# Optimization experiments

Hardware: AMD Instinct MI355X
Metric: run time of the kernel (lower is better)

Reference implementation:

```python
import jax, jax.numpy as jnp
import numpy as np
from jax import lax

N = 256        # graph nodes (== conv5 channels)
C = 128        # diff-pool clusters
E = 4096       # number of edges
EPS = 1e-15    # PyG dense_diff_pool entropy eps


def setup_inputs():
    key = jax.random.key(0)
    ks = jax.random.split(key, 24)
    def rn(k, shape, scale):
        return jax.random.normal(k, shape, dtype=jnp.float32) * scale
    inp = {
        "inputs": jax.random.normal(ks[0], (1, 3, 512, 512), dtype=jnp.float32),
        "edge_index": jax.random.randint(ks[1], (2, E), 0, N, dtype=jnp.int32),
    }
    convs = [(3, 32), (32, 64), (64, 128), (128, 256), (256, 256)]
    for i, (ci, co) in enumerate(convs):
        inp[f"w{i+1}"] = rn(ks[2 + i], (co, ci, 3, 3), 0.05)
        inp[f"b{i+1}"] = jnp.zeros((co,), jnp.float32)
    sages = [(256, 2), (256, 128), (2, 2)]
    for i, (ci, co) in enumerate(sages):
        inp[f"s{i+1}_wl"] = rn(ks[10 + 3 * i], (ci, co), 0.1)
        inp[f"s{i+1}_wr"] = rn(ks[11 + 3 * i], (ci, co), 0.1)
        inp[f"s{i+1}_b"] = jnp.zeros((co,), jnp.float32)
    return inp


def _conv_block(x, w, b):
    # 3x3 SAME conv -> relu -> 2x2 max pool (stride 2), NCHW layout
    x = lax.conv_general_dilated(x, w, (1, 1), 'SAME',
                                 dimension_numbers=('NCHW', 'OIHW', 'NCHW'))
    x = jax.nn.relu(x + b[None, :, None, None])
    return lax.reduce_window(x, -jnp.inf, lax.max,
                             (1, 1, 2, 2), (1, 1, 2, 2), 'VALID')


def _sage(x, src, dst, wl, wr, b, n):
    # PyG SAGEConv(normalize=False): lin_l(mean_{src->dst} x_src) + lin_r(x)
    tot = jax.ops.segment_sum(x[src], dst, num_segments=n)
    cnt = jax.ops.segment_sum(jnp.ones((dst.shape[0],), x.dtype), dst, num_segments=n)
    agg = jnp.where(cnt[:, None] > 0, tot / jnp.maximum(cnt, 1.0)[:, None], 0.0)
    return agg @ wl + b + x @ wr


def reference(inputs, edge_index, w1, b1, w2, b2, w3, b3, w4, b4, w5, b5,
              s1_wl, s1_wr, s1_b, s2_wl, s2_wr, s2_b, s3_wl, s3_wr, s3_b):
    x = inputs
    for w, b in ((w1, b1), (w2, b2), (w3, b3), (w4, b4), (w5, b5)):
        x = _conv_block(x, w, b)
    org = x.reshape(N, N)  # (256 channels, 16*16 spatial) -> node features
    src, dst = edge_index[0], edge_index[1]
    x1 = _sage(org, src, dst, s1_wl, s1_wr, s1_b, N)  # (256, 2)
    s = _sage(org, src, dst, s2_wl, s2_wr, s2_b, N)   # (256, 128)
    # dense adjacency (duplicate edges accumulate, matching scipy coo.todense())
    adj = jnp.zeros((N, N), org.dtype).at[src, dst].add(1.0)
    # dense_diff_pool
    s_soft = jax.nn.softmax(s, axis=-1)
    x_pool = s_soft.T @ x1               # (128, 2)
    adj_pool = s_soft.T @ adj @ s_soft   # (128, 128)
    link_loss = jnp.linalg.norm(adj - s_soft @ s_soft.T) / (N * N)
    ent_loss = (-s_soft * jnp.log(s_soft + EPS)).sum(-1).mean()
    nodes = jnp.tanh(x_pool)             # (128, 2)
    # per-row argmax-equality thresholding (vectorized: rows are independent)
    row_max = adj_pool.max(axis=1, keepdims=True)
    edge_bin = (adj_pool == row_max).astype(org.dtype)  # (128, 128)
    # sage3 over the binarized dense adjacency (equivalent to dense_to_sparse + SAGEConv)
    indeg = edge_bin.sum(axis=0)
    agg = jnp.where(indeg[:, None] > 0,
                    (edge_bin.T @ nodes) / jnp.maximum(indeg, 1.0)[:, None], 0.0)
    out = agg @ s3_wl + s3_b + nodes @ s3_wr  # (128, 2)
    return out.reshape(-1), link_loss, ent_loss, nodes, edge_bin
```

## Files before the change

kernel.cpp:

```cpp
#include <hip/hip_runtime.h>
#include <math.h>

#define NN 256
#define NE 4096
#define NC 128

using short8  = __attribute__((ext_vector_type(8))) short;
using short4v = __attribute__((ext_vector_type(4))) short;
using f32x4   = __attribute__((ext_vector_type(4))) float;

static __device__ __forceinline__ unsigned short f2bf(float x) {
    unsigned u = __float_as_uint(x);
    unsigned r = (u + 0x7FFF + ((u >> 16) & 1)) >> 16;
    return (unsigned short)r;
}

static __device__ __forceinline__ float block_sum_256(float v, float* red4) {
    #pragma unroll
    for (int o = 32; o > 0; o >>= 1) v += __shfl_xor(v, o);
    __syncthreads();
    if ((threadIdx.x & 63) == 0) red4[threadIdx.x >> 6] = v;
    __syncthreads();
    return (red4[0] + red4[1]) + (red4[2] + red4[3]);
}

__global__ void prep_kernel(const float* __restrict__ w1, const float* __restrict__ w2,
                            const float* __restrict__ w3, const float* __restrict__ w4,
                            const float* __restrict__ w5,
                            unsigned short* __restrict__ f1, unsigned short* __restrict__ f2,
                            unsigned short* __restrict__ f3, unsigned short* __restrict__ f4,
                            unsigned short* __restrict__ f5,
                            const int* __restrict__ src, const int* __restrict__ dst,
                            float* __restrict__ adj, float* __restrict__ adjT)
{
    int b = blockIdx.x;
    int tid = threadIdx.x;
    if (b >= 478) {
        __shared__ int cntA[256], cntT[256];
        const int n = b - 478;
        cntA[tid] = 0; cntT[tid] = 0;
        __syncthreads();
        #pragma unroll
        for (int i = 0; i < 16; ++i) {
            int e = tid + i * 256;
            int s = src[e], d = dst[e];
            if (s == n) atomicAdd(&cntA[d], 1);
            if (d == n) atomicAdd(&cntT[s], 1);
        }
        __syncthreads();
        adj[n * NN + tid]  = (float)cntA[tid];
        adjT[n * NN + tid] = (float)cntT[tid];
        return;
    }
    if (b == 477) {
        int lane = tid & 63, rest = tid >> 6;
        int g = rest & 1, slot = rest >> 1;
        int oc = g * 16 + (lane & 15);
        short8 v;
        #pragma unroll
        for (int j = 0; j < 8; ++j) {
            int k = (lane >> 4) * 8 + j;
            float wv = 0.f;
            if (slot == 0) {
                int tap = k >> 2, ch = k & 3;
                if (ch < 3) wv = w1[oc * 27 + ch * 9 + tap];
            } else {
                if (k < 3) wv = w1[oc * 27 + k * 9 + 8];
            }
            v[j] = (short)f2bf(wv);
        }
        *(short8*)&f1[(size_t)tid * 8] = v;
        return;
    }
    const float* w; unsigned short* f; int CIN, NG, NCH, base;
    if (b < 9)        { w = w2; f = f2; CIN = 32;  NG = 4;  NCH = 1; base = 0;   }
    else if (b < 45)  { w = w3; f = f3; CIN = 64;  NG = 8;  NCH = 2; base = 9;   }
    else if (b < 189) { w = w4; f = f4; CIN = 128; NG = 16; NCH = 4; base = 45;  }
    else              { w = w5; f = f5; CIN = 256; NG = 16; NCH = 8; base = 189; }
    int idx = (b - base) * 256 + tid;
    int lane = idx & 63, rest = idx >> 6;
    int c = rest % NCH; rest /= NCH;
    int g = rest % NG;  int t = rest / NG;
    if (t >= 9) return;
    int oc = g * 16 + (lane & 15);
    int cin0 = c * 32 + (lane >> 4) * 8;
    short8 v;
    #pragma unroll
    for (int j = 0; j < 8; ++j) {
        v[j] = (short)f2bf(w[((size_t)oc * CIN + cin0 + j) * 9 + t]);
    }
    *(short8*)&f[(size_t)idx * 8] = v;
}

__global__ __launch_bounds__(256) void conv1_kernel(
    const float* __restrict__ in, const unsigned short* __restrict__ wf1,
    const float* __restrict__ bias, unsigned short* __restrict__ out)
{
    constexpr int Hc = 512;
    const int tid = threadIdx.x;
    const int lane = tid & 63, wid = tid >> 6;
    const int col = lane & 15, kgl = lane >> 4;
    const int X0 = blockIdx.x * 16, Y0 = blockIdx.y * 16;
    __shared__ __align__(16) unsigned short lds[18][18][4];
    for (int i = tid; i < 324; i += 256) {
        int hy = i / 18, hx = i - hy * 18;
        int gy = Y0 + hy - 1, gx = X0 + hx - 1;
        float v0 = 0.f, v1 = 0.f, v2 = 0.f;
        if (gy >= 0 && gy < Hc && gx >= 0 && gx < Hc) {
            v0 = in[0 * 262144 + gy * 512 + gx];
            v1 = in[1 * 262144 + gy * 512 + gx];
            v2 = in[2 * 262144 + gy * 512 + gx];
        }
        uint2 uu;
        uu.x = f2bf(v0) | ((unsigned)f2bf(v1) << 16);
        uu.y = f2bf(v2);
        *(uint2*)&lds[hy][hx][0] = uu;
    }
    short8 af[2][2];
    #pragma unroll
    for (int slot = 0; slot < 2; ++slot) {
        #pragma unroll
        for (int g = 0; g < 2; ++g) {
            af[slot][g] = *(const short8*)&wf1[((size_t)((slot * 2 + g) * 64 + lane)) * 8];
        }
    }
    __syncthreads();
    f32x4 acc[2][4];
    #pragma unroll
    for (int g = 0; g < 2; ++g) {
        #pragma unroll
        for (int r = 0; r < 4; ++r) acc[g][r] = {0.f, 0.f, 0.f, 0.f};
    }
    const int t0 = 2 * kgl, t1 = 2 * kgl + 1;
    const int dy0 = t0 / 3, dx0 = t0 % 3, dy1 = t1 / 3, dx1 = t1 % 3;
    #pragma unroll
    for (int r = 0; r < 4; ++r) {
        const int py = wid * 4 + r;
        short4v lo = *(const short4v*)&lds[py + dy0][col + dx0][0];
        short4v hi = *(const short4v*)&lds[py + dy1][col + dx1][0];
        short8 bf0 = __builtin_shufflevector(lo, hi, 0, 1, 2, 3, 4, 5, 6, 7);
        short4v z4 = {0, 0, 0, 0};
        short4v t8 = z4;
        if (kgl == 0) t8 = *(const short4v*)&lds[py + 2][col + 2][0];
        short8 bf1 = __builtin_shufflevector(t8, z4, 0, 1, 2, 3, 4, 5, 6, 7);
        #pragma unroll
        for (int g = 0; g < 2; ++g) {
            acc[g][r] = __builtin_amdgcn_mfma_f32_16x16x32_bf16(af[0][g], bf0, acc[g][r], 0, 0, 0);
            acc[g][r] = __builtin_amdgcn_mfma_f32_16x16x32_bf16(af[1][g], bf1, acc[g][r], 0, 0, 0);
        }
    }
    #pragma unroll
    for (int g = 0; g < 2; ++g) {
        const int oc = g * 16 + kgl * 4;
        const float4 bb = *(const float4*)&bias[oc];
        const float bbv[4] = {bb.x, bb.y, bb.z, bb.w};
        #pragma unroll
        for (int pr = 0; pr < 2; ++pr) {
            float vv[4];
            #pragma unroll
            for (int q = 0; q < 4; ++q) {
                float v = fmaxf(acc[g][2 * pr][q], acc[g][2 * pr + 1][q]);
                v = fmaxf(v, __shfl_xor(v, 1));
                vv[q] = fmaxf(v + bbv[q], 0.f);
            }
            if (!(col & 1)) {
                unsigned u0 = f2bf(vv[0]) | ((unsigned)f2bf(vv[1]) << 16);
                unsigned u1 = f2bf(vv[2]) | ((unsigned)f2bf(vv[3]) << 16);
                const int pry = Y0 / 2 + wid * 2 + pr;
                const int prx = X0 / 2 + (col >> 1);
                uint2 uu; uu.x = u0; uu.y = u1;
                *(uint2*)&out[((size_t)(pry * 256 + prx)) * 32 + oc] = uu;
            }
        }
    }
}

template<int CIN, int COUT, int Hc, int OCB, int CSPLIT>
__global__ __launch_bounds__(256) void conv_mfma(
    const unsigned short* __restrict__ in, const unsigned short* __restrict__ wfrag,
    const float* __restrict__ bias, void* __restrict__ outv)
{
    constexpr int TR = 8;
    constexpr int NOG = OCB / 16;
    constexpr int NG  = COUT / 16;
    constexpr int NCHT = CIN / 32;
    constexpr int NCH = NCHT / CSPLIT;
    constexpr int RPW = 2;
    constexpr int ITEMS = (TR + 2) * 18 * 4;
    constexpr int NIT = 3;
    const int tid = threadIdx.x;
    const int lane = tid & 63, wid = tid >> 6;
    const int col = lane & 15, kgl = lane >> 4;
    const int X0 = blockIdx.x * 16, Y0 = blockIdx.y * TR;
    const int ob = blockIdx.z / CSPLIT, cs = blockIdx.z % CSPLIT;

    __shared__ __align__(16) unsigned short lds[2][ITEMS * 8];

    int ioff[NIT]; bool ival[NIT]; int loff[NIT];
    #pragma unroll
    for (int it = 0; it < NIT; ++it) {
        int i = tid + it * 256;
        int kg = i & 3, rem = i >> 2;
        int hx = rem % 18, hy = rem / 18;
        int gy = Y0 + hy - 1, gx = X0 + hx - 1;
        ival[it] = (i < ITEMS) && gy >= 0 && gy < Hc && gx >= 0 && gx < Hc;
        ioff[it] = (gy * Hc + gx) * CIN + kg * 8;
        loff[it] = ((hy * 4 + kg) * 18 + hx) * 8;
    }
    short8 sreg[NIT];
    auto sload = [&](int ca) {
        #pragma unroll
        for (int it = 0; it < NIT; ++it) {
            short8 v = {0, 0, 0, 0, 0, 0, 0, 0};
            if (ival[it]) v = *(const short8*)&in[ioff[it] + ca * 32];
            sreg[it] = v;
        }
    };
    auto swrite = [&](int buf) {
        #pragma unroll
        for (int it = 0; it < NIT; ++it) {
            if (tid + it * 256 < ITEMS) *(short8*)&lds[buf][loff[it]] = sreg[it];
        }
    };

    f32x4 acc[NOG][RPW];
    #pragma unroll
    for (int g = 0; g < NOG; ++g) {
        #pragma unroll
        for (int r = 0; r < RPW; ++r) acc[g][r] = {0.f, 0.f, 0.f, 0.f};
    }

    sload(cs * NCH);
    swrite(0);
    __syncthreads();
    for (int cc = 0; cc < NCH; ++cc) {
        const int ca = cs * NCH + cc;
        if (cc + 1 < NCH) sload(ca + 1);
        const unsigned short* L = &lds[cc & 1][0];
        #pragma unroll
        for (int t = 0; t < 9; ++t) {
            const int ky = t / 3, kx = t % 3;
            short8 af[NOG];
            #pragma unroll
            for (int g = 0; g < NOG; ++g) {
                af[g] = *(const short8*)&wfrag[((((size_t)t * NG + ob * NOG + g) * NCHT + ca) * 64 + lane) * 8];
            }
            #pragma unroll
            for (int r = 0; r < RPW; ++r) {
                const int py = wid * RPW + r;
                short8 bf = *(const short8*)&L[(((py + ky) * 4 + kgl) * 18 + col + kx) * 8];
                #pragma unroll
                for (int g = 0; g < NOG; ++g) {
                    acc[g][r] = __builtin_amdgcn_mfma_f32_16x16x32_bf16(af[g], bf, acc[g][r], 0, 0, 0);
                }
            }
        }
        if (cc + 1 < NCH) { swrite((cc + 1) & 1); __syncthreads(); }
    }

    if constexpr (CSPLIT == 1) {
        constexpr int Wp = Hc / 2;
        unsigned short* outp = (unsigned short*)outv;
        #pragma unroll
        for (int g = 0; g < NOG; ++g) {
            const int oc = (ob * NOG + g) * 16 + kgl * 4;
            const float4 bb = *(const float4*)&bias[oc];
            const float bbv[4] = {bb.x, bb.y, bb.z, bb.w};
            float vv[4];
            #pragma unroll
            for (int q = 0; q < 4; ++q) {
                float v = fmaxf(acc[g][0][q], acc[g][1][q]);
                v = fmaxf(v, __shfl_xor(v, 1));
                vv[q] = fmaxf(v + bbv[q], 0.f);
            }
            if (!(col & 1)) {
                unsigned u0 = f2bf(vv[0]) | ((unsigned)f2bf(vv[1]) << 16);
                unsigned u1 = f2bf(vv[2]) | ((unsigned)f2bf(vv[3]) << 16);
                const int pry = Y0 / 2 + wid;
                const int prx = X0 / 2 + (col >> 1);
                uint2 uu; uu.x = u0; uu.y = u1;
                *(uint2*)&outp[((size_t)(pry * Wp + prx)) * COUT + oc] = uu;
            }
        }
    } else {
        float* po = (float*)outv;
        #pragma unroll
        for (int g = 0; g < NOG; ++g) {
            #pragma unroll
            for (int r = 0; r < RPW; ++r) {
                const int gy = Y0 + wid * RPW + r;
                #pragma unroll
                for (int q = 0; q < 4; ++q) {
                    const int oc = (ob * NOG + g) * 16 + kgl * 4 + q;
                    po[((size_t)(cs * COUT + oc) * Hc + gy) * Hc + X0 + col] = acc[g][r][q];
                }
            }
        }
    }
}

template<int COUT, int HP, int CS>
__global__ void finalize_pool(const float* __restrict__ partial, const float* __restrict__ bias,
                              float* __restrict__ out)
{
    int idx = blockIdx.x * 256 + threadIdx.x;
    if (idx >= COUT * HP * HP) return;
    constexpr int H = HP * 2;
    int x = idx & (HP - 1); int rest = idx / HP;
    int y = rest & (HP - 1); int oc = rest / HP;
    float v00 = 0.f, v01 = 0.f, v10 = 0.f, v11 = 0.f;
    #pragma unroll
    for (int cs = 0; cs < CS; ++cs) {
        const float* p = partial + ((size_t)(cs * COUT + oc) * H + 2 * y) * H + 2 * x;
        v00 += p[0]; v01 += p[1]; v10 += p[H]; v11 += p[H + 1];
    }
    float m = fmaxf(fmaxf(v00, v01), fmaxf(v10, v11)) + bias[oc];
    out[idx] = fmaxf(m, 0.f);
}


__global__ __launch_bounds__(256) void node_fused_kernel(
    const float* __restrict__ adjT, const float* __restrict__ org,
    const float* __restrict__ s1wl, const float* __restrict__ s1wr, const float* __restrict__ s1b,
    const float* __restrict__ s2wl, const float* __restrict__ s2wr, const float* __restrict__ s2b,
    float* __restrict__ s_soft, float* __restrict__ s_softT,
    float* __restrict__ x1g, float* __restrict__ entp)
{
    int n = blockIdx.x, t = threadIdx.x;
    __shared__ float rowT[256], orgn[256], aggn[256], red[256], sm[128], red4[4];
    float rT = adjT[n * 256 + t];
    rowT[t] = rT; orgn[t] = org[n * 256 + t];
    __syncthreads();
    float cnt = block_sum_256(rT, red4);
    float a0 = 0.f, a1 = 0.f, a2 = 0.f, a3 = 0.f;
    #pragma unroll 8
    for (int s = 0; s < 256; s += 4) {
        a0 = fmaf(rowT[s + 0], org[(s + 0) * 256 + t], a0);
        a1 = fmaf(rowT[s + 1], org[(s + 1) * 256 + t], a1);
        a2 = fmaf(rowT[s + 2], org[(s + 2) * 256 + t], a2);
        a3 = fmaf(rowT[s + 3], org[(s + 3) * 256 + t], a3);
    }
    float acc = (a0 + a1) + (a2 + a3);
    float aggv = (cnt > 0.f) ? acc / cnt : 0.f;
    aggn[t] = aggv;
    float orgv = orgn[t];
    float x10 = block_sum_256(aggv * s1wl[2 * t] + orgv * s1wr[2 * t], red4) + s1b[0];
    float x11 = block_sum_256(aggv * s1wl[2 * t + 1] + orgv * s1wr[2 * t + 1], red4) + s1b[1];
    if (t == 0) { x1g[n * 2 + 0] = x10; x1g[n * 2 + 1] = x11; }
    int p = t & 127, h = t >> 7;
    float b0 = 0.f, b1 = 0.f, b2 = 0.f, b3 = 0.f;
    #pragma unroll 8
    for (int k = h * 128; k < h * 128 + 128; k += 2) {
        b0 = fmaf(aggn[k],     s2wl[k * NC + p],       b0);
        b1 = fmaf(orgn[k],     s2wr[k * NC + p],       b1);
        b2 = fmaf(aggn[k + 1], s2wl[(k + 1) * NC + p], b2);
        b3 = fmaf(orgn[k + 1], s2wr[(k + 1) * NC + p], b3);
    }
    red[t] = (b0 + b1) + (b2 + b3);
    __syncthreads();
    if (t < 128) sm[p] = red[t] + red[t + 128] + s2b[p];
    __syncthreads();
    if (t < 128) red[t] = sm[t];
    __syncthreads();
    for (int s = 64; s > 0; s >>= 1) { if (t < s) red[t] = fmaxf(red[t], red[t + s]); __syncthreads(); }
    float mx = red[0];
    __syncthreads();
    float e = 0.f;
    if (t < 128) { e = expf(sm[t] - mx); red[t] = e; } else { red[t] = 0.f; }
    __syncthreads();
    for (int s = 64; s > 0; s >>= 1) { if (t < s) red[t] += red[t + s]; __syncthreads(); }
    float denom = red[0];
    float q = e / denom;
    if (t < 128) {
        s_soft[n * NC + t] = q;
        s_softT[t * 256 + n] = q;
    }
    float ev = (t < 128) ? -q * logf(q + 1e-15f) : 0.f;
    float esum = block_sum_256(ev, red4);
    if (t == 0) entp[n] = esum;
}

__global__ __launch_bounds__(256) void row_fused_kernel(
    const float* __restrict__ adj, const float* __restrict__ s_soft,
    const float* __restrict__ s_softT, float* __restrict__ T, float* __restrict__ lpart)
{
    int i = blockIdx.x, j = threadIdx.x;
    __shared__ float si[NC], adjrow[256], tbuf[256], red4[4];
    adjrow[j] = adj[i * 256 + j];
    if (j < NC) si[j] = s_soft[i * NC + j];
    __syncthreads();
    float d0 = 0.f, d1 = 0.f, d2 = 0.f, d3 = 0.f;
    #pragma unroll 8
    for (int k = 0; k < NC; k += 4) {
        d0 = fmaf(si[k + 0], s_softT[(k + 0) * 256 + j], d0);
        d1 = fmaf(si[k + 1], s_softT[(k + 1) * 256 + j], d1);
        d2 = fmaf(si[k + 2], s_softT[(k + 2) * 256 + j], d2);
        d3 = fmaf(si[k + 3], s_softT[(k + 3) * 256 + j], d3);
    }
    float dot = (d0 + d1) + (d2 + d3);
    float dd = adjrow[j] - dot;
    float lsum = block_sum_256(dd * dd, red4);
    if (j == 0) lpart[i] = lsum;
    int p = j & 127, h = j >> 7;
    float a0 = 0.f, a1 = 0.f;
    #pragma unroll 8
    for (int k = h * 128; k < h * 128 + 128; k += 2) {
        a0 = fmaf(adjrow[k],     s_soft[k * NC + p],       a0);
        a1 = fmaf(adjrow[k + 1], s_soft[(k + 1) * NC + p], a1);
    }
    tbuf[j] = a0 + a1;
    __syncthreads();
    if (j < 128) T[i * NC + j] = tbuf[j] + tbuf[j + 128];
}

__global__ __launch_bounds__(256) void cluster_fused_kernel(
    const float* __restrict__ s_softT, const float* __restrict__ T, const float* __restrict__ x1g,
    float* __restrict__ eb_out, float* __restrict__ nodes_out)
{
    int c = blockIdx.x, t = threadIdx.x;
    __shared__ float colc[256], red[256], ap[NC], red4[4];
    colc[t] = s_softT[c * 256 + t];
    __syncthreads();
    int p = t & 127, h = t >> 7;
    float a0 = 0.f, a1 = 0.f;
    #pragma unroll 8
    for (int n = h * 128; n < h * 128 + 128; n += 2) {
        a0 = fmaf(colc[n],     T[n * NC + p],       a0);
        a1 = fmaf(colc[n + 1], T[(n + 1) * NC + p], a1);
    }
    red[t] = a0 + a1;
    __syncthreads();
    if (t < 128) ap[t] = red[t] + red[t + 128];
    __syncthreads();
    if (t < 128) red[t] = ap[t];
    __syncthreads();
    for (int s = 64; s > 0; s >>= 1) { if (t < s) red[t] = fmaxf(red[t], red[t + s]); __syncthreads(); }
    float mx = red[0];
    if (t < 128) eb_out[c * NC + t] = (ap[t] == mx) ? 1.f : 0.f;
    float n0 = tanhf(block_sum_256(colc[t] * x1g[t * 2 + 0], red4));
    float n1 = tanhf(block_sum_256(colc[t] * x1g[t * 2 + 1], red4));
    if (t == 0) { nodes_out[c * 2 + 0] = n0; nodes_out[c * 2 + 1] = n1; }
}

__global__ __launch_bounds__(256) void final_kernel(
    const float* __restrict__ lpart, const float* __restrict__ entp,
    const float* __restrict__ eb, const float* __restrict__ nodes,
    const float* __restrict__ wl, const float* __restrict__ wr, const float* __restrict__ b,
    float* __restrict__ out_main, float* __restrict__ out_link, float* __restrict__ out_ent)
{
    int t = threadIdx.x;
    __shared__ float red4[4];
    float ls = block_sum_256(lpart[t], red4);
    if (t == 0) out_link[0] = sqrtf(ls) / (float)(NN * NN);
    float es = block_sum_256(entp[t], red4);
    if (t == 0) out_ent[0] = es / (float)NN;
    if (t < NC) {
        int j = t;
        float i0 = 0.f, i1 = 0.f, a00 = 0.f, a01 = 0.f, a10 = 0.f, a11 = 0.f;
        #pragma unroll 8
        for (int i2 = 0; i2 < NC; i2 += 2) {
            float e0 = eb[i2 * NC + j];
            float e1 = eb[(i2 + 1) * NC + j];
            i0 += e0; i1 += e1;
            a00 = fmaf(e0, nodes[i2 * 2 + 0], a00);
            a01 = fmaf(e0, nodes[i2 * 2 + 1], a01);
            a10 = fmaf(e1, nodes[(i2 + 1) * 2 + 0], a10);
            a11 = fmaf(e1, nodes[(i2 + 1) * 2 + 1], a11);
        }
        float indeg = i0 + i1;
        float a0 = a00 + a10, a1 = a01 + a11;
        float inv = (indeg > 0.f) ? 1.f / fmaxf(indeg, 1.f) : 0.f;
        float g0 = a0 * inv, g1 = a1 * inv;
        float n0 = nodes[j * 2 + 0], n1 = nodes[j * 2 + 1];
        out_main[j * 2 + 0] = g0 * wl[0] + g1 * wl[2] + b[0] + n0 * wr[0] + n1 * wr[2];
        out_main[j * 2 + 1] = g0 * wl[1] + g1 * wl[3] + b[1] + n0 * wr[1] + n1 * wr[3];
    }
}

extern "C" void kernel_launch(void* const* d_in, const int* in_sizes, int n_in,
                              void* d_out, int out_size, void* d_ws, size_t ws_size,
                              hipStream_t stream)
{
    const float* input = (const float*)d_in[0];
    const int* eidx = (const int*)d_in[1];
    const int* src = eidx;
    const int* dst = eidx + NE;
    const float* w1 = (const float*)d_in[2];  const float* b1 = (const float*)d_in[3];
    const float* w2 = (const float*)d_in[4];  const float* b2 = (const float*)d_in[5];
    const float* w3 = (const float*)d_in[6];  const float* b3 = (const float*)d_in[7];
    const float* w4 = (const float*)d_in[8];  const float* b4 = (const float*)d_in[9];
    const float* w5 = (const float*)d_in[10]; const float* b5 = (const float*)d_in[11];
    const float* s1_wl = (const float*)d_in[12]; const float* s1_wr = (const float*)d_in[13];
    const float* s1_b  = (const float*)d_in[14];
    const float* s2_wl = (const float*)d_in[15]; const float* s2_wr = (const float*)d_in[16];
    const float* s2_b  = (const float*)d_in[17];
    const float* s3_wl = (const float*)d_in[18]; const float* s3_wr = (const float*)d_in[19];
    const float* s3_b  = (const float*)d_in[20];

    float* ws = (float*)d_ws;
    unsigned short* c1 = (unsigned short*)(ws);
    unsigned short* c2 = (unsigned short*)(ws + 1048576);
    unsigned short* c3 = (unsigned short*)(ws);
    unsigned short* c4 = (unsigned short*)(ws + 1048576);
    float* P5  = ws;
    float* ORG = ws + 1179648;
    unsigned short* f1 = (unsigned short*)(ws + 1572864);
    unsigned short* f2 = (unsigned short*)(ws + 1573888);
    unsigned short* f3 = (unsigned short*)(ws + 1583104);
    unsigned short* f4 = (unsigned short*)(ws + 1619968);
    unsigned short* f5 = (unsigned short*)(ws + 1767424);
    float* adj     = ws + 2062336;
    float* adjT    = ws + 2127872;
    float* s_soft  = ws + 2193408;
    float* T       = ws + 2226176;
    float* x1g     = ws + 2258944;
    float* lpart   = ws + 2259456;
    float* entp    = ws + 2259712;
    float* s_softT = ws + 2259968;

    float* fout = (float*)d_out;
    float* out_main  = fout;
    float* out_link  = fout + 256;
    float* out_ent   = fout + 257;
    float* out_nodes = fout + 258;
    float* out_eb    = fout + 514;

    prep_kernel<<<734, 256, 0, stream>>>(w1, w2, w3, w4, w5, f1, f2, f3, f4, f5,
                                         src, dst, adj, adjT);
    conv1_kernel<<<dim3(32, 32), 256, 0, stream>>>(input, f1, b1, c1);
    conv_mfma<32,  64, 256, 64, 1><<<dim3(16, 32, 1), 256, 0, stream>>>(c1, f2, b2, c2);
    conv_mfma<64, 128, 128, 64, 1><<<dim3(8, 16, 2),  256, 0, stream>>>(c2, f3, b3, c3);
    conv_mfma<128, 256, 64, 32, 1><<<dim3(4, 8, 8),   256, 0, stream>>>(c3, f4, b4, c4);
    conv_mfma<256, 256, 32, 16, 2><<<dim3(2, 4, 32),  256, 0, stream>>>(c4, f5, b5, P5);
    finalize_pool<256, 16, 2><<<256, 256, 0, stream>>>(P5, b5, ORG);

    node_fused_kernel<<<256, 256, 0, stream>>>(adjT, ORG, s1_wl, s1_wr, s1_b,
                                               s2_wl, s2_wr, s2_b, s_soft, s_softT, x1g, entp);
    row_fused_kernel<<<256, 256, 0, stream>>>(adj, s_soft, s_softT, T, lpart);
    cluster_fused_kernel<<<128, 256, 0, stream>>>(s_softT, T, x1g, out_eb, out_nodes);
    final_kernel<<<1, 256, 0, stream>>>(lpart, entp, out_eb, out_nodes,
                                        s3_wl, s3_wr, s3_b, out_main, out_link, out_ent);
}
```

Before: 107.7 us.

## Merge all stages into one cooperative persistent kernel with grid syncs

Replaces the eleven separate kernel launches with a single cooperative kernel of 256 blocks. Each stage loops over its former block indices and the stages are separated by grid-wide syncs. Shared memory becomes one union buffer reused by every stage. The goal is to remove per-launch overhead and inter-kernel gaps, at the cost of fixed parallelism (256 blocks, so conv1's 1024 tiles are serialized four per block), grid.sync overhead, and lower occupancy per stage.

```diff
diff --git a/kernel.cpp b/kernel.cpp
--- a/kernel.cpp
+++ b/kernel.cpp
@@ -1,5 +1,8 @@
 #include <hip/hip_runtime.h>
+#include <hip/hip_cooperative_groups.h>
 #include <math.h>
+
+namespace cg = cooperative_groups;
 
 #define NN 256
 #define NE 4096
@@ -24,32 +27,35 @@
     return (red4[0] + red4[1]) + (red4[2] + red4[3]);
 }
 
-__global__ void prep_kernel(const float* __restrict__ w1, const float* __restrict__ w2,
-                            const float* __restrict__ w3, const float* __restrict__ w4,
-                            const float* __restrict__ w5,
-                            unsigned short* __restrict__ f1, unsigned short* __restrict__ f2,
-                            unsigned short* __restrict__ f3, unsigned short* __restrict__ f4,
-                            unsigned short* __restrict__ f5,
-                            const int* __restrict__ src, const int* __restrict__ dst,
-                            float* __restrict__ adj, float* __restrict__ adjT)
-{
-    int b = blockIdx.x;
+struct MegaArgs {
+    const float* input; const int* src; const int* dst;
+    const float *w1, *b1, *w2, *b2, *w3, *b3, *w4, *b4, *w5, *b5;
+    const float *s1wl, *s1wr, *s1b, *s2wl, *s2wr, *s2b, *s3wl, *s3wr, *s3b;
+    unsigned short *c1, *c2, *c3, *c4, *f1, *f2, *f3, *f4, *f5;
+    float *P5, *ORG, *adj, *adjT, *s_soft, *s_softT, *T, *x1g, *lpart, *entp;
+    float *out_main, *out_link, *out_ent, *out_nodes, *out_eb;
+};
+
+static __device__ void prep_item(int b, const MegaArgs& a, int* icnt)
+{
     int tid = threadIdx.x;
     if (b >= 478) {
-        __shared__ int cntA[256], cntT[256];
+        int* cntA = icnt; int* cntT = icnt + 256;
         const int n = b - 478;
+        __syncthreads();
         cntA[tid] = 0; cntT[tid] = 0;
         __syncthreads();
         #pragma unroll
         for (int i = 0; i < 16; ++i) {
             int e = tid + i * 256;
-            int s = src[e], d = dst[e];
+            int s = a.src[e], d = a.dst[e];
             if (s == n) atomicAdd(&cntA[d], 1);
             if (d == n) atomicAdd(&cntT[s], 1);
         }
         __syncthreads();
-        adj[n * NN + tid]  = (float)cntA[tid];
-        adjT[n * NN + tid] = (float)cntT[tid];
+        a.adj[n * NN + tid]  = (float)cntA[tid];
+        a.adjT[n * NN + tid] = (float)cntT[tid];
+        __syncthreads();
         return;
     }
     if (b == 477) {
@@ -63,20 +69,20 @@
             float wv = 0.f;
             if (slot == 0) {
                 int tap = k >> 2, ch = k & 3;
-                if (ch < 3) wv = w1[oc * 27 + ch * 9 + tap];
+                if (ch < 3) wv = a.w1[oc * 27 + ch * 9 + tap];
             } else {
-                if (k < 3) wv = w1[oc * 27 + k * 9 + 8];
+                if (k < 3) wv = a.w1[oc * 27 + k * 9 + 8];
             }
             v[j] = (short)f2bf(wv);
         }
-        *(short8*)&f1[(size_t)tid * 8] = v;
+        *(short8*)&a.f1[(size_t)tid * 8] = v;
         return;
     }
     const float* w; unsigned short* f; int CIN, NG, NCH, base;
-    if (b < 9)        { w = w2; f = f2; CIN = 32;  NG = 4;  NCH = 1; base = 0;   }
-    else if (b < 45)  { w = w3; f = f3; CIN = 64;  NG = 8;  NCH = 2; base = 9;   }
-    else if (b < 189) { w = w4; f = f4; CIN = 128; NG = 16; NCH = 4; base = 45;  }
-    else              { w = w5; f = f5; CIN = 256; NG = 16; NCH = 8; base = 189; }
+    if (b < 9)        { w = a.w2; f = a.f2; CIN = 32;  NG = 4;  NCH = 1; base = 0;   }
+    else if (b < 45)  { w = a.w3; f = a.f3; CIN = 64;  NG = 8;  NCH = 2; base = 9;   }
+    else if (b < 189) { w = a.w4; f = a.f4; CIN = 128; NG = 16; NCH = 4; base = 45;  }
+    else              { w = a.w5; f = a.f5; CIN = 256; NG = 16; NCH = 8; base = 189; }
     int idx = (b - base) * 256 + tid;
     int lane = idx & 63, rest = idx >> 6;
     int c = rest % NCH; rest /= NCH;
@@ -92,36 +98,34 @@
     *(short8*)&f[(size_t)idx * 8] = v;
 }
 
-__global__ __launch_bounds__(256) void conv1_kernel(
-    const float* __restrict__ in, const unsigned short* __restrict__ wf1,
-    const float* __restrict__ bias, unsigned short* __restrict__ out)
+static __device__ void conv1_tile(int bx, int by, const MegaArgs& a, unsigned short* ldsb)
 {
     constexpr int Hc = 512;
     const int tid = threadIdx.x;
     const int lane = tid & 63, wid = tid >> 6;
     const int col = lane & 15, kgl = lane >> 4;
-    const int X0 = blockIdx.x * 16, Y0 = blockIdx.y * 16;
-    __shared__ __align__(16) unsigned short lds[18][18][4];
+    const int X0 = bx * 16, Y0 = by * 16;
+    __syncthreads();
     for (int i = tid; i < 324; i += 256) {
         int hy = i / 18, hx = i - hy * 18;
         int gy = Y0 + hy - 1, gx = X0 + hx - 1;
         float v0 = 0.f, v1 = 0.f, v2 = 0.f;
         if (gy >= 0 && gy < Hc && gx >= 0 && gx < Hc) {
-            v0 = in[0 * 262144 + gy * 512 + gx];
-            v1 = in[1 * 262144 + gy * 512 + gx];
-            v2 = in[2 * 262144 + gy * 512 + gx];
+            v0 = a.input[0 * 262144 + gy * 512 + gx];
+            v1 = a.input[1 * 262144 + gy * 512 + gx];
+            v2 = a.input[2 * 262144 + gy * 512 + gx];
         }
         uint2 uu;
         uu.x = f2bf(v0) | ((unsigned)f2bf(v1) << 16);
         uu.y = f2bf(v2);
-        *(uint2*)&lds[hy][hx][0] = uu;
+        *(uint2*)&ldsb[(size_t)i * 4] = uu;
     }
     short8 af[2][2];
     #pragma unroll
     for (int slot = 0; slot < 2; ++slot) {
         #pragma unroll
         for (int g = 0; g < 2; ++g) {
-            af[slot][g] = *(const short8*)&wf1[((size_t)((slot * 2 + g) * 64 + lane)) * 8];
+            af[slot][g] = *(const short8*)&a.f1[((size_t)((slot * 2 + g) * 64 + lane)) * 8];
         }
     }
     __syncthreads();
@@ -136,12 +140,12 @@
     #pragma unroll
     for (int r = 0; r < 4; ++r) {
         const int py = wid * 4 + r;
-        short4v lo = *(const short4v*)&lds[py + dy0][col + dx0][0];
-        short4v hi = *(const short4v*)&lds[py + dy1][col + dx1][0];
+        short4v lo = *(const short4v*)&ldsb[((py + dy0) * 18 + col + dx0) * 4];
+        short4v hi = *(const short4v*)&ldsb[((py + dy1) * 18 + col + dx1) * 4];
         short8 bf0 = __builtin_shufflevector(lo, hi, 0, 1, 2, 3, 4, 5, 6, 7);
         short4v z4 = {0, 0, 0, 0};
         short4v t8 = z4;
-        if (kgl == 0) t8 = *(const short4v*)&lds[py + 2][col + 2][0];
+        if (kgl == 0) t8 = *(const short4v*)&ldsb[((py + 2) * 18 + col + 2) * 4];
         short8 bf1 = __builtin_shufflevector(t8, z4, 0, 1, 2, 3, 4, 5, 6, 7);
         #pragma unroll
         for (int g = 0; g < 2; ++g) {
@@ -152,7 +156,7 @@
     #pragma unroll
     for (int g = 0; g < 2; ++g) {
         const int oc = g * 16 + kgl * 4;
-        const float4 bb = *(const float4*)&bias[oc];
+        const float4 bb = *(const float4*)&a.b1[oc];
         const float bbv[4] = {bb.x, bb.y, bb.z, bb.w};
         #pragma unroll
         for (int pr = 0; pr < 2; ++pr) {
@@ -169,16 +173,16 @@
                 const int pry = Y0 / 2 + wid * 2 + pr;
                 const int prx = X0 / 2 + (col >> 1);
                 uint2 uu; uu.x = u0; uu.y = u1;
-                *(uint2*)&out[((size_t)(pry * 256 + prx)) * 32 + oc] = uu;
+                *(uint2*)&a.c1[((size_t)(pry * 256 + prx)) * 32 + oc] = uu;
             }
         }
     }
 }
 
 template<int CIN, int COUT, int Hc, int OCB, int CSPLIT>
-__global__ __launch_bounds__(256) void conv_mfma(
+static __device__ void conv_tile(int bx, int by, int bz,
     const unsigned short* __restrict__ in, const unsigned short* __restrict__ wfrag,
-    const float* __restrict__ bias, void* __restrict__ outv)
+    const float* __restrict__ bias, void* __restrict__ outv, unsigned short* ldsb)
 {
     constexpr int TR = 8;
     constexpr int NOG = OCB / 16;
@@ -191,10 +195,8 @@
     const int tid = threadIdx.x;
     const int lane = tid & 63, wid = tid >> 6;
     const int col = lane & 15, kgl = lane >> 4;
-    const int X0 = blockIdx.x * 16, Y0 = blockIdx.y * TR;
-    const int ob = blockIdx.z / CSPLIT, cs = blockIdx.z % CSPLIT;
-
-    __shared__ __align__(16) unsigned short lds[2][ITEMS * 8];
+    const int X0 = bx * 16, Y0 = by * TR;
+    const int ob = bz / CSPLIT, cs = bz % CSPLIT;
 
     int ioff[NIT]; bool ival[NIT]; int loff[NIT];
     #pragma unroll
@@ -219,7 +221,7 @@
     auto swrite = [&](int buf) {
         #pragma unroll
         for (int it = 0; it < NIT; ++it) {
-            if (tid + it * 256 < ITEMS) *(short8*)&lds[buf][loff[it]] = sreg[it];
+            if (tid + it * 256 < ITEMS) *(short8*)&ldsb[buf * (ITEMS * 8) + loff[it]] = sreg[it];
         }
     };
 
@@ -230,13 +232,14 @@
         for (int r = 0; r < RPW; ++r) acc[g][r] = {0.f, 0.f, 0.f, 0.f};
     }
 
+    __syncthreads();
     sload(cs * NCH);
     swrite(0);
     __syncthreads();
     for (int cc = 0; cc < NCH; ++cc) {
         const int ca = cs * NCH + cc;
         if (cc + 1 < NCH) sload(ca + 1);
-        const unsigned short* L = &lds[cc & 1][0];
+        const unsigned short* L = &ldsb[(cc & 1) * (ITEMS * 8)];
         #pragma unroll
         for (int t = 0; t < 9; ++t) {
             const int ky = t / 3, kx = t % 3;
@@ -299,66 +302,59 @@
     }
 }
 
-template<int COUT, int HP, int CS>
-__global__ void finalize_pool(const float* __restrict__ partial, const float* __restrict__ bias,
-                              float* __restrict__ out)
-{
-    int idx = blockIdx.x * 256 + threadIdx.x;
-    if (idx >= COUT * HP * HP) return;
-    constexpr int H = HP * 2;
+static __device__ void finalize_item(int b, const MegaArgs& a)
+{
+    constexpr int HP = 16, H = 32, CS = 2, COUT = 256;
+    int idx = b * 256 + threadIdx.x;
     int x = idx & (HP - 1); int rest = idx / HP;
     int y = rest & (HP - 1); int oc = rest / HP;
     float v00 = 0.f, v01 = 0.f, v10 = 0.f, v11 = 0.f;
     #pragma unroll
     for (int cs = 0; cs < CS; ++cs) {
-        const float* p = partial + ((size_t)(cs * COUT + oc) * H + 2 * y) * H + 2 * x;
+        const float* p = a.P5 + ((size_t)(cs * COUT + oc) * H + 2 * y) * H + 2 * x;
         v00 += p[0]; v01 += p[1]; v10 += p[H]; v11 += p[H + 1];
     }
-    float m = fmaxf(fmaxf(v00, v01), fmaxf(v10, v11)) + bias[oc];
-    out[idx] = fmaxf(m, 0.f);
-}
-
-
-__global__ __launch_bounds__(256) void node_fused_kernel(
-    const float* __restrict__ adjT, const float* __restrict__ org,
-    const float* __restrict__ s1wl, const float* __restrict__ s1wr, const float* __restrict__ s1b,
-    const float* __restrict__ s2wl, const float* __restrict__ s2wr, const float* __restrict__ s2b,
-    float* __restrict__ s_soft, float* __restrict__ s_softT,
-    float* __restrict__ x1g, float* __restrict__ entp)
-{
-    int n = blockIdx.x, t = threadIdx.x;
-    __shared__ float rowT[256], orgn[256], aggn[256], red[256], sm[128], red4[4];
-    float rT = adjT[n * 256 + t];
-    rowT[t] = rT; orgn[t] = org[n * 256 + t];
+    float m = fmaxf(fmaxf(v00, v01), fmaxf(v10, v11)) + a.b5[oc];
+    a.ORG[idx] = fmaxf(m, 0.f);
+}
+
+static __device__ void node_tile(int n, const MegaArgs& a, float* sf)
+{
+    int t = threadIdx.x;
+    float* rowT = sf; float* orgn = sf + 256; float* aggn = sf + 512;
+    float* red = sf + 768; float* sm = sf + 1024; float* red4 = sf + 1152;
+    __syncthreads();
+    float rT = a.adjT[n * 256 + t];
+    rowT[t] = rT; orgn[t] = a.ORG[n * 256 + t];
     __syncthreads();
     float cnt = block_sum_256(rT, red4);
     float a0 = 0.f, a1 = 0.f, a2 = 0.f, a3 = 0.f;
     #pragma unroll 8
     for (int s = 0; s < 256; s += 4) {
-        a0 = fmaf(rowT[s + 0], org[(s + 0) * 256 + t], a0);
-        a1 = fmaf(rowT[s + 1], org[(s + 1) * 256 + t], a1);
-        a2 = fmaf(rowT[s + 2], org[(s + 2) * 256 + t], a2);
-        a3 = fmaf(rowT[s + 3], org[(s + 3) * 256 + t], a3);
+        a0 = fmaf(rowT[s + 0], a.ORG[(s + 0) * 256 + t], a0);
+        a1 = fmaf(rowT[s + 1], a.ORG[(s + 1) * 256 + t], a1);
+        a2 = fmaf(rowT[s + 2], a.ORG[(s + 2) * 256 + t], a2);
+        a3 = fmaf(rowT[s + 3], a.ORG[(s + 3) * 256 + t], a3);
     }
     float acc = (a0 + a1) + (a2 + a3);
     float aggv = (cnt > 0.f) ? acc / cnt : 0.f;
     aggn[t] = aggv;
     float orgv = orgn[t];
-    float x10 = block_sum_256(aggv * s1wl[2 * t] + orgv * s1wr[2 * t], red4) + s1b[0];
-    float x11 = block_sum_256(aggv * s1wl[2 * t + 1] + orgv * s1wr[2 * t + 1], red4) + s1b[1];
-    if (t == 0) { x1g[n * 2 + 0] = x10; x1g[n * 2 + 1] = x11; }
+    float x10 = block_sum_256(aggv * a.s1wl[2 * t] + orgv * a.s1wr[2 * t], red4) + a.s1b[0];
+    float x11 = block_sum_256(aggv * a.s1wl[2 * t + 1] + orgv * a.s1wr[2 * t + 1], red4) + a.s1b[1];
+    if (t == 0) { a.x1g[n * 2 + 0] = x10; a.x1g[n * 2 + 1] = x11; }
     int p = t & 127, h = t >> 7;
     float b0 = 0.f, b1 = 0.f, b2 = 0.f, b3 = 0.f;
     #pragma unroll 8
     for (int k = h * 128; k < h * 128 + 128; k += 2) {
-        b0 = fmaf(aggn[k],     s2wl[k * NC + p],       b0);
-        b1 = fmaf(orgn[k],     s2wr[k * NC + p],       b1);
-        b2 = fmaf(aggn[k + 1], s2wl[(k + 1) * NC + p], b2);
-        b3 = fmaf(orgn[k + 1], s2wr[(k + 1) * NC + p], b3);
+        b0 = fmaf(aggn[k],     a.s2wl[k * NC + p],       b0);
+        b1 = fmaf(orgn[k],     a.s2wr[k * NC + p],       b1);
+        b2 = fmaf(aggn[k + 1], a.s2wl[(k + 1) * NC + p], b2);
+        b3 = fmaf(orgn[k + 1], a.s2wr[(k + 1) * NC + p], b3);
     }
     red[t] = (b0 + b1) + (b2 + b3);
     __syncthreads();
-    if (t < 128) sm[p] = red[t] + red[t + 128] + s2b[p];
+    if (t < 128) sm[p] = red[t] + red[t + 128] + a.s2b[p];
     __syncthreads();
     if (t < 128) red[t] = sm[t];
     __syncthreads();
@@ -372,61 +368,59 @@
     float denom = red[0];
     float q = e / denom;
     if (t < 128) {
-        s_soft[n * NC + t] = q;
-        s_softT[t * 256 + n] = q;
+        a.s_soft[n * NC + t] = q;
+        a.s_softT[t * 256 + n] = q;
     }
     float ev = (t < 128) ? -q * logf(q + 1e-15f) : 0.f;
     float esum = block_sum_256(ev, red4);
-    if (t == 0) entp[n] = esum;
-}
-
-__global__ __launch_bounds__(256) void row_fused_kernel(
-    const float* __restrict__ adj, const float* __restrict__ s_soft,
-    const float* __restrict__ s_softT, float* __restrict__ T, float* __restrict__ lpart)
-{
-    int i = blockIdx.x, j = threadIdx.x;
-    __shared__ float si[NC], adjrow[256], tbuf[256], red4[4];
-    adjrow[j] = adj[i * 256 + j];
-    if (j < NC) si[j] = s_soft[i * NC + j];
+    if (t == 0) a.entp[n] = esum;
+}
+
+static __device__ void row_tile(int i, const MegaArgs& a, float* sf)
+{
+    int j = threadIdx.x;
+    float* si = sf; float* adjrow = sf + 128; float* tbuf = sf + 384; float* red4 = sf + 640;
+    __syncthreads();
+    adjrow[j] = a.adj[i * 256 + j];
+    if (j < NC) si[j] = a.s_soft[i * NC + j];
     __syncthreads();
     float d0 = 0.f, d1 = 0.f, d2 = 0.f, d3 = 0.f;
     #pragma unroll 8
     for (int k = 0; k < NC; k += 4) {
-        d0 = fmaf(si[k + 0], s_softT[(k + 0) * 256 + j], d0);
-        d1 = fmaf(si[k + 1], s_softT[(k + 1) * 256 + j], d1);
-        d2 = fmaf(si[k + 2], s_softT[(k + 2) * 256 + j], d2);
-        d3 = fmaf(si[k + 3], s_softT[(k + 3) * 256 + j], d3);
+        d0 = fmaf(si[k + 0], a.s_softT[(k + 0) * 256 + j], d0);
+        d1 = fmaf(si[k + 1], a.s_softT[(k + 1) * 256 + j], d1);
+        d2 = fmaf(si[k + 2], a.s_softT[(k + 2) * 256 + j], d2);
+        d3 = fmaf(si[k + 3], a.s_softT[(k + 3) * 256 + j], d3);
     }
     float dot = (d0 + d1) + (d2 + d3);
     float dd = adjrow[j] - dot;
     float lsum = block_sum_256(dd * dd, red4);
-    if (j == 0) lpart[i] = lsum;
+    if (j == 0) a.lpart[i] = lsum;
     int p = j & 127, h = j >> 7;
     float a0 = 0.f, a1 = 0.f;
     #pragma unroll 8
     for (int k = h * 128; k < h * 128 + 128; k += 2) {
-        a0 = fmaf(adjrow[k],     s_soft[k * NC + p],       a0);
-        a1 = fmaf(adjrow[k + 1], s_soft[(k + 1) * NC + p], a1);
+        a0 = fmaf(adjrow[k],     a.s_soft[k * NC + p],       a0);
+        a1 = fmaf(adjrow[k + 1], a.s_soft[(k + 1) * NC + p], a1);
     }
     tbuf[j] = a0 + a1;
     __syncthreads();
-    if (j < 128) T[i * NC + j] = tbuf[j] + tbuf[j + 128];
-}
-
-__global__ __launch_bounds__(256) void cluster_fused_kernel(
-    const float* __restrict__ s_softT, const float* __restrict__ T, const float* __restrict__ x1g,
-    float* __restrict__ eb_out, float* __restrict__ nodes_out)
-{
-    int c = blockIdx.x, t = threadIdx.x;
-    __shared__ float colc[256], red[256], ap[NC], red4[4];
-    colc[t] = s_softT[c * 256 + t];
+    if (j < 128) a.T[i * NC + j] = tbuf[j] + tbuf[j + 128];
+}
+
+static __device__ void cluster_tile(int c, const MegaArgs& a, float* sf)
+{
+    int t = threadIdx.x;
+    float* colc = sf; float* red = sf + 256; float* ap = sf + 512; float* red4 = sf + 640;
+    __syncthreads();
+    colc[t] = a.s_softT[c * 256 + t];
     __syncthreads();
     int p = t & 127, h = t >> 7;
     float a0 = 0.f, a1 = 0.f;
     #pragma unroll 8
     for (int n = h * 128; n < h * 128 + 128; n += 2) {
-        a0 = fmaf(colc[n],     T[n * NC + p],       a0);
-        a1 = fmaf(colc[n + 1], T[(n + 1) * NC + p], a1);
+        a0 = fmaf(colc[n],     a.T[n * NC + p],       a0);
+        a1 = fmaf(colc[n + 1], a.T[(n + 1) * NC + p], a1);
     }
     red[t] = a0 + a1;
     __syncthreads();
@@ -436,108 +430,126 @@
     __syncthreads();
     for (int s = 64; s > 0; s >>= 1) { if (t < s) red[t] = fmaxf(red[t], red[t + s]); __syncthreads(); }
     float mx = red[0];
-    if (t < 128) eb_out[c * NC + t] = (ap[t] == mx) ? 1.f : 0.f;
-    float n0 = tanhf(block_sum_256(colc[t] * x1g[t * 2 + 0], red4));
-    float n1 = tanhf(block_sum_256(colc[t] * x1g[t * 2 + 1], red4));
-    if (t == 0) { nodes_out[c * 2 + 0] = n0; nodes_out[c * 2 + 1] = n1; }
-}
-
-__global__ __launch_bounds__(256) void final_kernel(
-    const float* __restrict__ lpart, const float* __restrict__ entp,
-    const float* __restrict__ eb, const float* __restrict__ nodes,
-    const float* __restrict__ wl, const float* __restrict__ wr, const float* __restrict__ b,
-    float* __restrict__ out_main, float* __restrict__ out_link, float* __restrict__ out_ent)
+    if (t < 128) a.out_eb[c * NC + t] = (ap[t] == mx) ? 1.f : 0.f;
+    float n0 = tanhf(block_sum_256(colc[t] * a.x1g[t * 2 + 0], red4));
+    float n1 = tanhf(block_sum_256(colc[t] * a.x1g[t * 2 + 1], red4));
+    if (t == 0) { a.out_nodes[c * 2 + 0] = n0; a.out_nodes[c * 2 + 1] = n1; }
+}
+
+static __device__ void final_tile(const MegaArgs& a, float* sf)
 {
     int t = threadIdx.x;
-    __shared__ float red4[4];
-    float ls = block_sum_256(lpart[t], red4);
-    if (t == 0) out_link[0] = sqrtf(ls) / (float)(NN * NN);
-    float es = block_sum_256(entp[t], red4);
-    if (t == 0) out_ent[0] = es / (float)NN;
+    float* red4 = sf;
+    __syncthreads();
+    float ls = block_sum_256(a.lpart[t], red4);
+    if (t == 0) a.out_link[0] = sqrtf(ls) / (float)(NN * NN);
+    float es = block_sum_256(a.entp[t], red4);
+    if (t == 0) a.out_ent[0] = es / (float)NN;
     if (t < NC) {
         int j = t;
         float i0 = 0.f, i1 = 0.f, a00 = 0.f, a01 = 0.f, a10 = 0.f, a11 = 0.f;
         #pragma unroll 8
         for (int i2 = 0; i2 < NC; i2 += 2) {
-            float e0 = eb[i2 * NC + j];
-            float e1 = eb[(i2 + 1) * NC + j];
+            float e0 = a.out_eb[i2 * NC + j];
+            float e1 = a.out_eb[(i2 + 1) * NC + j];
             i0 += e0; i1 += e1;
-            a00 = fmaf(e0, nodes[i2 * 2 + 0], a00);
-            a01 = fmaf(e0, nodes[i2 * 2 + 1], a01);
-            a10 = fmaf(e1, nodes[(i2 + 1) * 2 + 0], a10);
-            a11 = fmaf(e1, nodes[(i2 + 1) * 2 + 1], a11);
+            a00 = fmaf(e0, a.out_nodes[i2 * 2 + 0], a00);
+            a01 = fmaf(e0, a.out_nodes[i2 * 2 + 1], a01);
+            a10 = fmaf(e1, a.out_nodes[(i2 + 1) * 2 + 0], a10);
+            a11 = fmaf(e1, a.out_nodes[(i2 + 1) * 2 + 1], a11);
         }
         float indeg = i0 + i1;
         float a0 = a00 + a10, a1 = a01 + a11;
         float inv = (indeg > 0.f) ? 1.f / fmaxf(indeg, 1.f) : 0.f;
         float g0 = a0 * inv, g1 = a1 * inv;
-        float n0 = nodes[j * 2 + 0], n1 = nodes[j * 2 + 1];
-        out_main[j * 2 + 0] = g0 * wl[0] + g1 * wl[2] + b[0] + n0 * wr[0] + n1 * wr[2];
-        out_main[j * 2 + 1] = g0 * wl[1] + g1 * wl[3] + b[1] + n0 * wr[1] + n1 * wr[3];
-    }
+        float n0 = a.out_nodes[j * 2 + 0], n1 = a.out_nodes[j * 2 + 1];
+        a.out_main[j * 2 + 0] = g0 * a.s3wl[0] + g1 * a.s3wl[2] + a.s3b[0] + n0 * a.s3wr[0] + n1 * a.s3wr[2];
+        a.out_main[j * 2 + 1] = g0 * a.s3wl[1] + g1 * a.s3wl[3] + a.s3b[1] + n0 * a.s3wr[1] + n1 * a.s3wr[3];
+    }
+}
+
+__global__ __launch_bounds__(256) void mega_kernel(MegaArgs a)
+{
+    cg::grid_group grid = cg::this_grid();
+    __shared__ __align__(16) unsigned char smem_[23040];
+    unsigned short* ldsb = (unsigned short*)smem_;
+    float* sf = (float*)smem_;
+    const int nb = gridDim.x;
+
+    for (int b = blockIdx.x; b < 734; b += nb) prep_item(b, a, (int*)smem_);
+    grid.sync();
+    for (int b = blockIdx.x; b < 1024; b += nb) conv1_tile(b & 31, b >> 5, a, ldsb);
+    grid.sync();
+    for (int b = blockIdx.x; b < 512; b += nb)
+        conv_tile<32, 64, 256, 64, 1>(b & 15, b >> 4, 0, a.c1, a.f2, a.b2, a.c2, ldsb);
+    grid.sync();
+    for (int b = blockIdx.x; b < 256; b += nb)
+        conv_tile<64, 128, 128, 64, 1>(b & 7, (b >> 3) & 15, b >> 7, a.c2, a.f3, a.b3, a.c3, ldsb);
+    grid.sync();
+    for (int b = blockIdx.x; b < 256; b += nb)
+        conv_tile<128, 256, 64, 32, 1>(b & 3, (b >> 2) & 7, b >> 5, a.c3, a.f4, a.b4, a.c4, ldsb);
+    grid.sync();
+    for (int b = blockIdx.x; b < 256; b += nb)
+        conv_tile<256, 256, 32, 16, 2>(b & 1, (b >> 1) & 3, b >> 3, a.c4, a.f5, a.b5, a.P5, ldsb);
+    grid.sync();
+    for (int b = blockIdx.x; b < 256; b += nb) finalize_item(b, a);
+    grid.sync();
+    for (int b = blockIdx.x; b < 256; b += nb) node_tile(b, a, sf);
+    grid.sync();
+    for (int b = blockIdx.x; b < 256; b += nb) row_tile(b, a, sf);
+    grid.sync();
+    for (int b = blockIdx.x; b < 128; b += nb) cluster_tile(b, a, sf);
+    grid.sync();
+    if (blockIdx.x == 0) final_tile(a, sf);
 }
 
 extern "C" void kernel_launch(void* const* d_in, const int* in_sizes, int n_in,
                               void* d_out, int out_size, void* d_ws, size_t ws_size,
                               hipStream_t stream)
 {
-    const float* input = (const float*)d_in[0];
     const int* eidx = (const int*)d_in[1];
-    const int* src = eidx;
-    const int* dst = eidx + NE;
-    const float* w1 = (const float*)d_in[2];  const float* b1 = (const float*)d_in[3];
-    const float* w2 = (const float*)d_in[4];  const float* b2 = (const float*)d_in[5];
-    const float* w3 = (const float*)d_in[6];  const float* b3 = (const float*)d_in[7];
-    const float* w4 = (const float*)d_in[8];  const float* b4 = (const float*)d_in[9];
-    const float* w5 = (const float*)d_in[10]; const float* b5 = (const float*)d_in[11];
-    const float* s1_wl = (const float*)d_in[12]; const float* s1_wr = (const float*)d_in[13];
-    const float* s1_b  = (const float*)d_in[14];
-    const float* s2_wl = (const float*)d_in[15]; const float* s2_wr = (const float*)d_in[16];
-    const float* s2_b  = (const float*)d_in[17];
-    const float* s3_wl = (const float*)d_in[18]; const float* s3_wr = (const float*)d_in[19];
-    const float* s3_b  = (const float*)d_in[20];
-
     float* ws = (float*)d_ws;
-    unsigned short* c1 = (unsigned short*)(ws);
-    unsigned short* c2 = (unsigned short*)(ws + 1048576);
-    unsigned short* c3 = (unsigned short*)(ws);
-    unsigned short* c4 = (unsigned short*)(ws + 1048576);
-    float* P5  = ws;
-    float* ORG = ws + 1179648;
-    unsigned short* f1 = (unsigned short*)(ws + 1572864);
-    unsigned short* f2 = (unsigned short*)(ws + 1573888);
-    unsigned short* f3 = (unsigned short*)(ws + 1583104);
-    unsigned short* f4 = (unsigned short*)(ws + 1619968);
-    unsigned short* f5 = (unsigned short*)(ws + 1767424);
-    float* adj     = ws + 2062336;
-    float* adjT    = ws + 2127872;
-    float* s_soft  = ws + 2193408;
-    float* T       = ws + 2226176;
-    float* x1g     = ws + 2258944;
-    float* lpart   = ws + 2259456;
-    float* entp    = ws + 2259712;
-    float* s_softT = ws + 2259968;
-
     float* fout = (float*)d_out;
-    float* out_main  = fout;
-    float* out_link  = fout + 256;
-    float* out_ent   = fout + 257;
-    float* out_nodes = fout + 258;
-    float* out_eb    = fout + 514;
-
-    prep_kernel<<<734, 256, 0, stream>>>(w1, w2, w3, w4, w5, f1, f2, f3, f4, f5,
-                                         src, dst, adj, adjT);
-    conv1_kernel<<<dim3(32, 32), 256, 0, stream>>>(input, f1, b1, c1);
-    conv_mfma<32,  64, 256, 64, 1><<<dim3(16, 32, 1), 256, 0, stream>>>(c1, f2, b2, c2);
-    conv_mfma<64, 128, 128, 64, 1><<<dim3(8, 16, 2),  256, 0, stream>>>(c2, f3, b3, c3);
-    conv_mfma<128, 256, 64, 32, 1><<<dim3(4, 8, 8),   256, 0, stream>>>(c3, f4, b4, c4);
-    conv_mfma<256, 256, 32, 16, 2><<<dim3(2, 4, 32),  256, 0, stream>>>(c4, f5, b5, P5);
-    finalize_pool<256, 16, 2><<<256, 256, 0, stream>>>(P5, b5, ORG);
-
-    node_fused_kernel<<<256, 256, 0, stream>>>(adjT, ORG, s1_wl, s1_wr, s1_b,
-                                               s2_wl, s2_wr, s2_b, s_soft, s_softT, x1g, entp);
-    row_fused_kernel<<<256, 256, 0, stream>>>(adj, s_soft, s_softT, T, lpart);
-    cluster_fused_kernel<<<128, 256, 0, stream>>>(s_softT, T, x1g, out_eb, out_nodes);
-    final_kernel<<<1, 256, 0, stream>>>(lpart, entp, out_eb, out_nodes,
-                                        s3_wl, s3_wr, s3_b, out_main, out_link, out_ent);
-}
+
+    MegaArgs a;
+    a.input = (const float*)d_in[0];
+    a.src = eidx; a.dst = eidx + NE;
+    a.w1 = (const float*)d_in[2];  a.b1 = (const float*)d_in[3];
+    a.w2 = (const float*)d_in[4];  a.b2 = (const float*)d_in[5];
+    a.w3 = (const float*)d_in[6];  a.b3 = (const float*)d_in[7];
+    a.w4 = (const float*)d_in[8];  a.b4 = (const float*)d_in[9];
+    a.w5 = (const float*)d_in[10]; a.b5 = (const float*)d_in[11];
+    a.s1wl = (const float*)d_in[12]; a.s1wr = (const float*)d_in[13]; a.s1b = (const float*)d_in[14];
+    a.s2wl = (const float*)d_in[15]; a.s2wr = (const float*)d_in[16]; a.s2b = (const float*)d_in[17];
+    a.s3wl = (const float*)d_in[18]; a.s3wr = (const float*)d_in[19]; a.s3b = (const float*)d_in[20];
+
+    a.c1 = (unsigned short*)(ws);
+    a.c2 = (unsigned short*)(ws + 1048576);
+    a.c3 = (unsigned short*)(ws);
+    a.c4 = (unsigned short*)(ws + 1048576);
+    a.P5 = ws;
+    a.ORG = ws + 1179648;
+    a.f1 = (unsigned short*)(ws + 1572864);
+    a.f2 = (unsigned short*)(ws + 1573888);
+    a.f3 = (unsigned short*)(ws + 1583104);
+    a.f4 = (unsigned short*)(ws + 1619968);
+    a.f5 = (unsigned short*)(ws + 1767424);
+    a.adj = ws + 2062336;
+    a.adjT = ws + 2127872;
+    a.s_soft = ws + 2193408;
+    a.T = ws + 2226176;
+    a.x1g = ws + 2258944;
+    a.lpart = ws + 2259456;
+    a.entp = ws + 2259712;
+    a.s_softT = ws + 2259968;
+
+    a.out_main = fout;
+    a.out_link = fout + 256;
+    a.out_ent = fout + 257;
+    a.out_nodes = fout + 258;
+    a.out_eb = fout + 514;
+
+    void* kargs[] = { (void*)&a };
+    hipLaunchCooperativeKernel((const void*)mega_kernel, dim3(256), dim3(256),
+                               kargs, 0, stream);
+}
```

New measurement: 366.8 us. 3.41x slower.
